# Kernel optimization log

Hardware: AMD Instinct MI355X
Metric: run time of the kernel (lower is better)

Reference implementation:

```python
import jax, jax.numpy as jnp
import numpy as np
from jax import lax

N_SEEDS = 16
N_SAMPS = 32
IN_C = 3
HID = [32, 64, 64]
K = 3
H = W = 64
EPS = 1e-5


def _uniform(key, shape, bound):
    return jax.random.uniform(key, shape, jnp.float32, -bound, bound)


def setup_inputs() -> dict:
    key = jax.random.key(0)
    keys = jax.random.split(key, 32)
    inp = {"x": jax.random.normal(keys[0], (N_SEEDS, N_SAMPS, IN_C, H, W), jnp.float32)}
    c_in = IN_C
    ki = 1
    for li, c_out in enumerate(HID, start=1):
        fan_in = c_in * K * K
        # kaiming_uniform with a=sqrt(5): gain=sqrt(2/(1+5))=sqrt(1/3); bound=sqrt(3)*gain/sqrt(fan)=1/sqrt(fan)
        wb = 1.0 / np.sqrt(fan_in)
        inp[f"w{li}"] = _uniform(keys[ki], (N_SEEDS * c_out, c_in, K, K), wb); ki += 1
        inp[f"b{li}"] = _uniform(keys[ki], (N_SEEDS * c_out,), wb); ki += 1
        inp[f"g{li}"] = jnp.ones((N_SEEDS * c_out,), jnp.float32)
        inp[f"be{li}"] = jnp.zeros((N_SEEDS * c_out,), jnp.float32)
        c_in = c_out
    return inp


def _layer(h, w, b, g, be):
    # grouped conv: groups = N_SEEDS, OIHW weights, NCHW data, stride 1, pad 1
    h = lax.conv_general_dilated(
        h, w, window_strides=(1, 1), padding=((1, 1), (1, 1)),
        feature_group_count=N_SEEDS,
        dimension_numbers=("NCHW", "OIHW", "NCHW"))
    h = h + b[None, :, None, None]
    # BatchNorm2d, training mode: batch statistics over (N, H, W), biased variance
    mean = jnp.mean(h, axis=(0, 2, 3))
    var = jnp.var(h, axis=(0, 2, 3))
    h = (h - mean[None, :, None, None]) * (g / jnp.sqrt(var + EPS))[None, :, None, None] + be[None, :, None, None]
    return jax.nn.relu(h)


def reference(x, w1, b1, g1, be1, w2, b2, g2, be2, w3, b3, g3, be3):
    S, N, C, Hh, Ww = x.shape  # (n_seeds, n_samps, C, H, W)
    h = jnp.swapaxes(x, 0, 1).reshape(N, S * C, Hh, Ww)
    h = _layer(h, w1, b1, g1, be1)
    h = _layer(h, w2, b2, g2, be2)
    h = _layer(h, w3, b3, g3, be3)
    c_out = HID[-1]
    h = h.reshape(N, S, c_out, Hh, Ww)
    return jnp.swapaxes(h, 0, 1)  # (n_seeds, n_samps, C_out, H, W)
```

## Files before the change

kernel.cpp:

```cpp
#include <hip/hip_runtime.h>
#include <cstddef>
#include <cstdint>

typedef __attribute__((ext_vector_type(8))) _Float16 half8;
typedef __attribute__((ext_vector_type(4))) _Float16 half4;
typedef __attribute__((ext_vector_type(4))) float f32x4;
typedef _Float16 half_t;

#define NS 16
#define NN 32

static const size_t OFF_H1P = 0;
static const size_t OFF_H3  = 138412032ull;
static const size_t OFF_ZR1 = 138412032ull + 276824064ull;
static const size_t OFF_ZR2 = OFF_ZR1 + 67584ull;
static const size_t OFF_WT1 = OFF_ZR2 + 135168ull;
static const size_t OFF_WT2 = OFF_WT1 + 55296ull;
static const size_t OFF_WT3 = OFF_WT2 + 589824ull;
static const size_t OFF_SUMS = OFF_WT3 + 1179648ull;
static const size_t OFF_PRM = OFF_SUMS + 20480ull;
static const size_t OFF_TH  = OFF_PRM + 30720ull;

static __device__ __forceinline__ half8 sr8(half8 v, half8 t) {
    half8 r = v + t;
    half8 z = {};
#if defined(__has_builtin) && __has_builtin(__builtin_elementwise_max)
    return __builtin_elementwise_max(r, z);
#else
#pragma unroll
    for (int j = 0; j < 8; ++j) r[j] = r[j] > (_Float16)0 ? r[j] : (_Float16)0;
    return r;
#endif
}

__global__ __launch_bounds__(256) void transform1_k(
    const float* __restrict__ w1, float* __restrict__ wt1)
{
    int idx = blockIdx.x * 256 + threadIdx.x;
    if (idx >= 13824) return;
    int o = idx & 31, tap = (idx >> 5) % 9, ic = (idx / 288) % 3, s = idx / 864;
    wt1[idx] = w1[((s * 32 + o) * 3 + ic) * 9 + tap];
}

__global__ __launch_bounds__(256) void wtrans2_k(
    const float* __restrict__ w2, const float* __restrict__ a1, half_t* __restrict__ wt2)
{
    int idx = blockIdx.x * 256 + threadIdx.x;
    if (idx >= 294912) return;
    int ic = idx & 31, oc = (idx >> 5) & 63, tap = (idx >> 11) % 9, s = idx / 18432;
    wt2[idx] = (half_t)(w2[((s * 64 + oc) * 32 + ic) * 9 + tap] * a1[s * 32 + ic]);
}

__global__ __launch_bounds__(256) void wtrans3_k(
    const float* __restrict__ w3, const float* __restrict__ a2, half_t* __restrict__ wt3)
{
    int idx = blockIdx.x * 256 + threadIdx.x;
    if (idx >= 589824) return;
    int ic = idx & 63, oc = (idx >> 6) & 63, tap = (idx >> 12) % 9, s = idx / 36864;
    wt3[idx] = (half_t)(w3[((s * 64 + oc) * 64 + ic) * 9 + tap] * a2[s * 64 + ic]);
}

__global__ __launch_bounds__(256) void conv1_k(
    const float* __restrict__ x, const float* __restrict__ wt1,
    const float* __restrict__ b1, half_t* __restrict__ h1p,
    float* __restrict__ sums1)
{
    __shared__ float smem[8512];
    float* xt = smem;
    float* bounce = smem;
    float* statsl = smem + 8448;
    const int tile = blockIdx.x, s = blockIdx.y, n = blockIdx.z;
    const int tx = tile & 3, ty = tile >> 2, tid = threadIdx.x;

    for (int i = tid; i < 972; i += 256) {
        int ic = i / 324, rem = i - ic * 324;
        int py = rem / 18, px = rem - py * 18;
        int gy = ty * 16 + py - 1, gx = tx * 16 + px - 1;
        float v = 0.f;
        if ((unsigned)gy < 64u && (unsigned)gx < 64u)
            v = x[(size_t)(((s * NN + n) * 3 + ic) * 64 + gy) * 64 + gx];
        xt[i] = v;
    }
    if (tid < 64) statsl[tid] = 0.f;
    __syncthreads();

    const int px = tid & 15, py = tid >> 4;
    float acc[32];
#pragma unroll
    for (int o = 0; o < 32; ++o) acc[o] = 0.f;
#pragma unroll
    for (int ic = 0; ic < 3; ++ic)
#pragma unroll
        for (int ky = 0; ky < 3; ++ky)
#pragma unroll
            for (int kx = 0; kx < 3; ++kx) {
                float v = xt[ic * 324 + (py + ky) * 18 + px + kx];
                const float* wp = wt1 + ((s * 3 + ic) * 9 + ky * 3 + kx) * 32;
#pragma unroll
                for (int o = 0; o < 32; ++o) acc[o] = fmaf(wp[o], v, acc[o]);
            }
    const float* bp = b1 + s * 32;
#pragma unroll
    for (int o = 0; o < 32; ++o) acc[o] += bp[o];

    const int gy1 = ty * 16 + py, gxp = tx * 16 + px + 1;
    half8* dst = (half8*)(h1p + (size_t)(n * NS + s) * 135168 + (size_t)(gy1 * 66 + gxp) * 32);
#pragma unroll
    for (int k = 0; k < 4; ++k) {
        half8 v8;
#pragma unroll
        for (int j = 0; j < 8; ++j) v8[j] = (half_t)acc[k * 8 + j];
        dst[k] = v8;
    }
    __syncthreads();
#pragma unroll
    for (int o = 0; o < 32; ++o) bounce[tid * 33 + o] = acc[o];
    __syncthreads();
    {
        const int oc = tid & 31, grp = tid >> 5;
        float s1 = 0.f, s2 = 0.f;
#pragma unroll 4
        for (int jj = 0; jj < 32; ++jj) {
            float v = bounce[(grp * 32 + jj) * 33 + oc];
            s1 += v; s2 += v * v;
        }
        atomicAdd(&statsl[oc * 2], s1);
        atomicAdd(&statsl[oc * 2 + 1], s2);
    }
    __syncthreads();
    if (tid < 64)
        atomicAdd(&sums1[(s * 32 + (tid >> 1)) * 2 + (tid & 1)], statsl[tid]);
}

__global__ void bnparam_k(const float* __restrict__ sums, const float* __restrict__ g,
                          const float* __restrict__ be, float* __restrict__ a,
                          float* __restrict__ b, float* __restrict__ t,
                          half_t* __restrict__ th, int C)
{
    int ch = blockIdx.x * 256 + threadIdx.x;
    if (ch >= C) return;
    const float inv = 1.f / 131072.f;
    float mean = sums[ch * 2] * inv;
    float var = sums[ch * 2 + 1] * inv - mean * mean;
    float sc = g[ch] * rsqrtf(var + 1e-5f);
    a[ch] = sc;
    float bb = be[ch] - mean * sc;
    b[ch] = bb;
    float tt = bb / sc;
    t[ch] = tt;
    th[ch] = (half_t)tt;
}

__global__ __launch_bounds__(256) void padfill_k(
    half_t* __restrict__ img, half_t* __restrict__ zrow, const float* __restrict__ t,
    int C, int c8shift, long imgstride, int rowstride, long tot_cols, long tot)
{
    long idx = (long)blockIdx.x * 256 + threadIdx.x;
    if (idx >= tot) return;
    const int nc8m = (1 << c8shift) - 1;
    if (idx < tot_cols) {
        int c8 = (int)idx & nc8m; long r = idx >> c8shift;
        int side = (int)r & 1; r >>= 1;
        int y = (int)r & 63; r >>= 6;
        int si = (int)(r & 15); int ni = (int)(r >> 4);
        half8 q;
#pragma unroll
        for (int j = 0; j < 8; ++j) q[j] = (half_t)(-(t[si * C + c8 * 8 + j] + 1.0f));
        *(half8*)(img + (long)(ni * NS + si) * imgstride + (long)y * rowstride +
                  (side ? 65 : 0) * C + c8 * 8) = q;
    } else {
        long r2 = idx - tot_cols;
        int c8 = (int)r2 & nc8m; r2 >>= c8shift;
        int xx = (int)(r2 % 66); int si = (int)(r2 / 66);
        half8 q;
#pragma unroll
        for (int j = 0; j < 8; ++j) q[j] = (half_t)(-(t[si * C + c8 * 8 + j] + 1.0f));
        *(half8*)(zrow + ((long)(si * 66 + xx)) * C + c8 * 8) = q;
    }
}

__device__ __forceinline__ void loadB2(half8 bf[4], const half_t* wb, int tap, int l15, int g) {
#pragma unroll
    for (int nt = 0; nt < 4; ++nt)
        bf[nt] = *(const half8*)(wb + (tap * 64 + nt * 16 + l15) * 32 + g * 8);
}

__device__ __forceinline__ void comp2(f32x4 acc[4][4], const half8 bf[4], const char* smem,
                                      int tap, int wv, int l15, int g) {
    const int ky = tap / 3, kx = tap - ky * 3;
#pragma unroll
    for (int mt = 0; mt < 4; ++mt) {
        int p = (wv * 4 + mt + ky) * 18 + l15 + kx;
        half8 av = *(const half8*)(smem + p * 80 + g * 16);
#pragma unroll
        for (int nt = 0; nt < 4; ++nt)
            acc[mt][nt] = __builtin_amdgcn_mfma_f32_16x16x32_f16(av, bf[nt], acc[mt][nt], 0, 0, 0);
    }
}

__global__ __launch_bounds__(256, 3) void conv2_k(
    const half_t* __restrict__ h1p, const half_t* __restrict__ zr1,
    const half_t* __restrict__ wt2, const float* __restrict__ b2,
    const half_t* __restrict__ th1, half_t* __restrict__ h2p,
    float* __restrict__ sums2)
{
    __shared__ __align__(16) char smem[37376];
    float* statsl = (float*)(smem + 36864);
    const int tile = blockIdx.x, s = blockIdx.y, n = blockIdx.z;
    const int tx = tile & 3, ty = tile >> 2, tid = threadIdx.x;
    const int l = tid & 63, wv = tid >> 6, l15 = l & 15, g = l >> 4;
    if (tid < 128) statsl[tid] = 0.f;

    const half_t* wb = wt2 + (size_t)s * 18432;
    half8 bfa[4], bfb[4];
    loadB2(bfa, wb, 0, l15, g);

    const half_t* img = h1p + (size_t)(n * NS + s) * 135168;
    const half_t* zrow = zr1 + s * 2112;
    const int j = tid & 3;
    const half8 tshj = *(const half8*)(th1 + s * 32 + j * 8);
    for (int i = tid; i < 1296; i += 256) {
        int p = i >> 2;
        int py = p / 18, pxx = p - py * 18;
        int gy = ty * 16 + py - 1;
        const half_t* rp = ((unsigned)gy < 64u) ? (img + (size_t)gy * 2112) : zrow;
        half8 v = sr8(*(const half8*)(rp + (tx * 16 + pxx) * 32 + j * 8), tshj);
        *(half8*)(smem + p * 80 + j * 16) = v;
    }
    __syncthreads();

    f32x4 acc[4][4];
#pragma unroll
    for (int mt = 0; mt < 4; ++mt)
#pragma unroll
        for (int nt = 0; nt < 4; ++nt) acc[mt][nt] = (f32x4){0.f, 0.f, 0.f, 0.f};

#pragma unroll
    for (int tap = 0; tap < 9; ++tap) {
        if (tap & 1) {
            if (tap < 8) loadB2(bfa, wb, tap + 1, l15, g);
            comp2(acc, bfb, smem, tap, wv, l15, g);
        } else {
            if (tap < 8) loadB2(bfb, wb, tap + 1, l15, g);
            comp2(acc, bfa, smem, tap, wv, l15, g);
        }
    }

    float s1a[4], s2a[4];
#pragma unroll
    for (int nt = 0; nt < 4; ++nt) {
        float bias = b2[s * 64 + nt * 16 + l15];
        float s1 = 0.f, s2 = 0.f;
#pragma unroll
        for (int mt = 0; mt < 4; ++mt)
#pragma unroll
            for (int r = 0; r < 4; ++r) {
                float v = acc[mt][nt][r] + bias;
                acc[mt][nt][r] = v;
                s1 += v; s2 += v * v;
            }
        s1 += __shfl_xor(s1, 16); s1 += __shfl_xor(s1, 32);
        s2 += __shfl_xor(s2, 16); s2 += __shfl_xor(s2, 32);
        s1a[nt] = s1; s2a[nt] = s2;
    }
    if (l < 16) {
#pragma unroll
        for (int nt = 0; nt < 4; ++nt) {
            atomicAdd(&statsl[(nt * 16 + l15) * 2], s1a[nt]);
            atomicAdd(&statsl[(nt * 16 + l15) * 2 + 1], s2a[nt]);
        }
    }
    __syncthreads();

    half_t* obuf = (half_t*)smem;
#pragma unroll
    for (int mt = 0; mt < 4; ++mt)
#pragma unroll
        for (int nt = 0; nt < 4; ++nt)
#pragma unroll
            for (int r = 0; r < 4; ++r)
                obuf[((wv * 4 + mt) * 16 + g * 4 + r) * 72 + nt * 16 + l15] = (half_t)acc[mt][nt][r];
    __syncthreads();

    half_t* img2 = h2p + (size_t)(n * NS + s) * 270336;
    for (int i = tid; i < 2048; i += 256) {
        int p = i >> 3, cc = i & 7;
        int y = ty * 16 + (p >> 4), xp = tx * 16 + (p & 15) + 1;
        *(half8*)(img2 + (size_t)y * 4224 + xp * 64 + cc * 8) = *(const half8*)(obuf + p * 72 + cc * 8);
    }
    if (tid < 128)
        atomicAdd(&sums2[(s * 64 + (tid >> 1)) * 2 + (tid & 1)], statsl[tid]);
}

__global__ __launch_bounds__(512, 4) void conv3_k(
    const half_t* __restrict__ h2p, const half_t* __restrict__ zr2,
    const half_t* __restrict__ wt3, const float* __restrict__ b3,
    const half_t* __restrict__ th2, half_t* __restrict__ h3,
    float* __restrict__ sums3)
{
    __shared__ __align__(16) char smem[51200];
    float* statsl = (float*)(smem + 50688);
    const int ty = blockIdx.x, s = blockIdx.y, n = blockIdx.z;
    const int tid = threadIdx.x;
    const int l = tid & 63, w = tid >> 6, l15 = l & 15, g = l >> 4;
    const int wy = w & 3, och = w >> 2;
    const int ty4 = ty * 4;
    if (tid < 128) statsl[tid] = 0.f;

    const half_t* img = h2p + (size_t)(n * NS + s) * 270336;
    const half_t* zrow = zr2 + s * 4224;
    const half_t* wb = wt3 + (size_t)s * 36864;
    const int j = tid & 7;
    const half8 tshj = *(const half8*)(th2 + s * 64 + j * 8);

    half8 sa0, sa1, sa2, sa3, sa4; int aa0, aa1, aa2, aa3, aa4;
#define PREPA(K, ST, SL) { int idx = tid + K * 512; int p = idx >> 3; int rr = p / 66; \
    int col = p - rr * 66; int row = ty4 - 1 + rr; bool ok = idx < 2112; \
    const half_t* rp = ((unsigned)row < 64u) ? (img + (size_t)row * 4224) : zrow; \
    ST = *(const half8*)(rp + col * 64 + j * 8); \
    SL = ok ? (rr * 8448 + col * 128 + ((j * 16) ^ ((col & 7) << 4))) : -1; }
    PREPA(0, sa0, aa0)
    PREPA(1, sa1, aa1)
    PREPA(2, sa2, aa2)
    PREPA(3, sa3, aa3)
    PREPA(4, sa4, aa4)
#undef PREPA
    half8 sb0, sb1, sb2; int ab0, ab1, ab2;
#define PREPB(K, ST, SL) { int idx = tid + K * 512; int p = idx >> 3; int rr = p / 66; \
    int col = p - rr * 66; int row = ty4 + 3 + rr; bool ok = idx < 1056; \
    const half_t* rp = ((unsigned)row < 64u) ? (img + (size_t)row * 4224) : zrow; \
    ST = *(const half8*)(rp + col * 64 + j * 8); \
    SL = ok ? ((4 + rr) * 8448 + col * 128 + ((j * 16) ^ ((col & 7) << 4))) : -1; }
    PREPB(0, sb0, ab0)
    PREPB(1, sb1, ab1)
    PREPB(2, sb2, ab2)
#undef PREPB
    if (aa0 >= 0) *(half8*)(smem + aa0) = sr8(sa0, tshj);
    if (aa1 >= 0) *(half8*)(smem + aa1) = sr8(sa1, tshj);
    if (aa2 >= 0) *(half8*)(smem + aa2) = sr8(sa2, tshj);
    if (aa3 >= 0) *(half8*)(smem + aa3) = sr8(sa3, tshj);
    if (aa4 >= 0) *(half8*)(smem + aa4) = sr8(sa4, tshj);
    __syncthreads();

    f32x4 acc[4][2];
#pragma unroll
    for (int mt = 0; mt < 4; ++mt)
#pragma unroll
        for (int nt = 0; nt < 2; ++nt) acc[mt][nt] = (f32x4){0.f, 0.f, 0.f, 0.f};

    const int UT[19] = {0,1,2,0,1,2, 3,4,5,6,7,8, 3,4,5,6,7,8, 0};
    const int UK[19] = {0,0,0,1,1,1, 0,0,0,0,0,0, 1,1,1,1,1,1, 0};
    half8 bfa[2], bfb[2], bfc[2];
#define LW3(BF, U) { \
    BF[0] = *(const half8*)(wb + (UT[U] * 64 + och * 32 + l15) * 64 + UK[U] * 32 + g * 8); \
    BF[1] = *(const half8*)(wb + (UT[U] * 64 + och * 32 + 16 + l15) * 64 + UK[U] * 32 + g * 8); }
    LW3(bfa, 0)
    LW3(bfb, 1)
#define CSTEP3(BF, U) { \
    int tap_ = UT[U]; int ky_ = tap_ / 3, kx_ = tap_ - ky_ * 3; \
    const char* rp_ = smem + (wy + ky_) * 8448; \
    _Pragma("unroll") \
    for (int mt = 0; mt < 4; ++mt) { \
        int px = mt * 16 + l15 + kx_; \
        int sw = (px & 7) << 4; \
        half8 a_ = *(const half8*)(rp_ + px * 128 + ((UK[U] * 64 + g * 16) ^ sw)); \
        acc[mt][0] = __builtin_amdgcn_mfma_f32_16x16x32_f16(a_, BF[0], acc[mt][0], 0, 0, 0); \
        acc[mt][1] = __builtin_amdgcn_mfma_f32_16x16x32_f16(a_, BF[1], acc[mt][1], 0, 0, 0); \
    } }

    LW3(bfc, 2)  CSTEP3(bfa, 0)
    LW3(bfa, 3)  CSTEP3(bfb, 1)
    LW3(bfb, 4)  CSTEP3(bfc, 2)
    LW3(bfc, 5)  CSTEP3(bfa, 3)
    LW3(bfa, 6)  CSTEP3(bfb, 4)
    LW3(bfb, 7)  CSTEP3(bfc, 5)
    if (ab0 >= 0) *(half8*)(smem + ab0) = sr8(sb0, tshj);
    if (ab1 >= 0) *(half8*)(smem + ab1) = sr8(sb1, tshj);
    if (ab2 >= 0) *(half8*)(smem + ab2) = sr8(sb2, tshj);
    __syncthreads();
    LW3(bfc, 8)   CSTEP3(bfa, 6)
    LW3(bfa, 9)   CSTEP3(bfb, 7)
    LW3(bfb, 10)  CSTEP3(bfc, 8)
    LW3(bfc, 11)  CSTEP3(bfa, 9)
    LW3(bfa, 12)  CSTEP3(bfb, 10)
    LW3(bfb, 13)  CSTEP3(bfc, 11)
    LW3(bfc, 14)  CSTEP3(bfa, 12)
    LW3(bfa, 15)  CSTEP3(bfb, 13)
    LW3(bfb, 16)  CSTEP3(bfc, 14)
    LW3(bfc, 17)  CSTEP3(bfa, 15)
                  CSTEP3(bfb, 16)
                  CSTEP3(bfc, 17)
#undef CSTEP3
#undef LW3

    float bias0 = b3[s * 64 + och * 32 + l15];
    float bias1 = b3[s * 64 + och * 32 + 16 + l15];
    float s10 = 0.f, s20 = 0.f, s11 = 0.f, s21 = 0.f;
    const int gy = ty4 + wy;
    half_t* hb = h3 + (size_t)((s * NN + n) * 64) * 4096;
#pragma unroll
    for (int mt = 0; mt < 4; ++mt)
#pragma unroll
        for (int nt = 0; nt < 2; ++nt) {
            int c = och * 32 + nt * 16 + l15;
            float bias = nt ? bias1 : bias0;
            half4 hv;
#pragma unroll
            for (int r = 0; r < 4; ++r) {
                float vv = acc[mt][nt][r] + bias;
                hv[r] = (half_t)vv;
                if (nt) { s11 += vv; s21 += vv * vv; } else { s10 += vv; s20 += vv * vv; }
            }
            *(half4*)(hb + (size_t)c * 4096 + gy * 64 + mt * 16 + g * 4) = hv;
        }

    s10 += __shfl_xor(s10, 16); s10 += __shfl_xor(s10, 32);
    s20 += __shfl_xor(s20, 16); s20 += __shfl_xor(s20, 32);
    s11 += __shfl_xor(s11, 16); s11 += __shfl_xor(s11, 32);
    s21 += __shfl_xor(s21, 16); s21 += __shfl_xor(s21, 32);
    if (l < 16) {
        atomicAdd(&statsl[(och * 32 + l15) * 2], s10);
        atomicAdd(&statsl[(och * 32 + l15) * 2 + 1], s20);
        atomicAdd(&statsl[(och * 32 + 16 + l15) * 2], s11);
        atomicAdd(&statsl[(och * 32 + 16 + l15) * 2 + 1], s21);
    }
    __syncthreads();
    if (tid < 128)
        atomicAdd(&sums3[(s * 64 + (tid >> 1)) * 2 + (tid & 1)], statsl[tid]);
}

__global__ __launch_bounds__(256) void final_k(float* __restrict__ out,
                                               const half_t* __restrict__ h3,
                                               const float* __restrict__ a3,
                                               const float* __restrict__ b3p)
{
    const size_t stride = (size_t)gridDim.x * 256;
    for (size_t i = (size_t)blockIdx.x * 256 + threadIdx.x; i < 16777216ull; i += stride) {
        size_t e = i * 8;
        int ch = (int)((e >> 12) & 63) + (int)(e >> 23) * 64;
        float sc = a3[ch], sh = b3p[ch];
        half8 hv = *(const half8*)(h3 + e);
        f32x4 v0, v1;
#pragma unroll
        for (int r = 0; r < 4; ++r) {
            v0[r] = fmaxf(fmaf(sc, (float)hv[r], sh), 0.f);
            v1[r] = fmaxf(fmaf(sc, (float)hv[r + 4], sh), 0.f);
        }
        *(f32x4*)(out + e) = v0;
        *(f32x4*)(out + e + 4) = v1;
    }
}

extern "C" void kernel_launch(void* const* d_in, const int* in_sizes, int n_in,
                              void* d_out, int out_size, void* d_ws, size_t ws_size,
                              hipStream_t stream)
{
    const float* x   = (const float*)d_in[0];
    const float* w1  = (const float*)d_in[1];
    const float* b1  = (const float*)d_in[2];
    const float* g1  = (const float*)d_in[3];
    const float* be1 = (const float*)d_in[4];
    const float* w2  = (const float*)d_in[5];
    const float* b2  = (const float*)d_in[6];
    const float* g2  = (const float*)d_in[7];
    const float* be2 = (const float*)d_in[8];
    const float* w3  = (const float*)d_in[9];
    const float* b3  = (const float*)d_in[10];
    const float* g3  = (const float*)d_in[11];
    const float* be3 = (const float*)d_in[12];

    char* ws = (char*)d_ws;
    half_t* h1p = (half_t*)(ws + OFF_H1P);
    half_t* h2p = (half_t*)d_out;
    half_t* h3  = (half_t*)(ws + OFF_H3);
    half_t* zr1 = (half_t*)(ws + OFF_ZR1);
    half_t* zr2 = (half_t*)(ws + OFF_ZR2);
    float*  wt1 = (float*)(ws + OFF_WT1);
    half_t* wt2 = (half_t*)(ws + OFF_WT2);
    half_t* wt3 = (half_t*)(ws + OFF_WT3);
    float*  sums = (float*)(ws + OFF_SUMS);
    float *s1v = sums, *s2v = sums + 1024, *s3v = sums + 3072;
    float*  prm = (float*)(ws + OFF_PRM);
    float *a1 = prm,        *b1p = prm + 512,  *t1 = prm + 1024;
    float *a2 = prm + 1536, *b2p = prm + 2560, *t2 = prm + 3584;
    float *a3 = prm + 4608, *b3p = prm + 5632, *t3 = prm + 6656;
    half_t* th = (half_t*)(ws + OFF_TH);
    half_t *th1 = th, *th2 = th + 512, *th3 = th + 1536;
    float* out = (float*)d_out;

    hipMemsetAsync(ws + OFF_SUMS, 0, 20480, stream);
    transform1_k<<<54, 256, 0, stream>>>(w1, wt1);
    dim3 grid1(16, 16, 32);
    conv1_k<<<grid1, 256, 0, stream>>>(x, wt1, b1, h1p, s1v);
    bnparam_k<<<2, 256, 0, stream>>>(s1v, g1, be1, a1, b1p, t1, th1, 512);
    padfill_k<<<1041, 256, 0, stream>>>(h1p, zr1, t1, 32, 2, 135168L, 2112, 262144L, 266368L);
    wtrans2_k<<<1152, 256, 0, stream>>>(w2, a1, wt2);
    conv2_k<<<grid1, 256, 0, stream>>>(h1p, zr1, wt2, b2, th1, h2p, s2v);
    bnparam_k<<<4, 256, 0, stream>>>(s2v, g2, be2, a2, b2p, t2, th2, 1024);
    padfill_k<<<2081, 256, 0, stream>>>(h2p, zr2, t2, 64, 3, 270336L, 4224, 524288L, 532736L);
    wtrans3_k<<<2304, 256, 0, stream>>>(w3, a2, wt3);
    dim3 grid3(16, 16, 32);
    conv3_k<<<grid3, 512, 0, stream>>>(h2p, zr2, wt3, b3, th2, h3, s3v);
    bnparam_k<<<4, 256, 0, stream>>>(s3v, g3, be3, a3, b3p, t3, th3, 1024);
    final_k<<<4096, 256, 0, stream>>>(out, h3, a3, b3p);
}
```

Before: 848.4 us.

## Pipeline conv3 over 16-row strips with async global-to-LDS ring buffer

conv3 now handles a 16-row strip per block, four 4-row steps in all, instead of one 4-row tile. Input rows stream into a 9-row LDS ring through global_load_lds direct copies that overlap the MFMA work. The XOR swizzle moves into the global h2 layout (conv2 stores and padfill) so the raw 16-byte copies land already swizzled, and the BN shift plus ReLU is applied when the data is read from LDS. This cuts halo reloads and register staging, at the cost of more LDS per block (lower occupancy), fewer blocks, and repeated sr8 work on every A-fragment read.

```diff
diff --git a/kernel.cpp b/kernel.cpp
--- a/kernel.cpp
+++ b/kernel.cpp
@@ -31,6 +31,22 @@
     for (int j = 0; j < 8; ++j) r[j] = r[j] > (_Float16)0 ? r[j] : (_Float16)0;
     return r;
 #endif
+}
+
+typedef __attribute__((address_space(1))) const void gas_t;
+typedef __attribute__((address_space(3))) void las_t;
+static __device__ __forceinline__ void gl16(const void* g, void* l) {
+    __builtin_amdgcn_global_load_lds((gas_t*)g, (las_t*)l, 16, 0, 0);
+}
+
+static __device__ __forceinline__ void stage_row3(const half_t* __restrict__ img,
+                                                  const half_t* __restrict__ zrow,
+                                                  char* smem, int r, int w, int lane) {
+    const char* src = (const char*)(((unsigned)r < 64u) ? (img + (size_t)r * 4224) : zrow)
+                      + (size_t)w * 1056;
+    char* dst = smem + (size_t)((unsigned)(r + 18) % 9u) * 8448 + w * 1056;
+    gl16(src + lane * 16, dst + lane * 16);
+    if (lane < 2) gl16(src + 1024 + lane * 16, dst + 1024 + lane * 16);
 }
 
 __global__ __launch_bounds__(256) void transform1_k(
@@ -153,7 +169,7 @@
 
 __global__ __launch_bounds__(256) void padfill_k(
     half_t* __restrict__ img, half_t* __restrict__ zrow, const float* __restrict__ t,
-    int C, int c8shift, long imgstride, int rowstride, long tot_cols, long tot)
+    int C, int c8shift, long imgstride, int rowstride, long tot_cols, long tot, int swz)
 {
     long idx = (long)blockIdx.x * 256 + threadIdx.x;
     if (idx >= tot) return;
@@ -166,8 +182,10 @@
         half8 q;
 #pragma unroll
         for (int j = 0; j < 8; ++j) q[j] = (half_t)(-(t[si * C + c8 * 8 + j] + 1.0f));
+        int col = side ? 65 : 0;
+        int off = swz ? ((c8 * 8) ^ ((col & 7) << 3)) : (c8 * 8);
         *(half8*)(img + (long)(ni * NS + si) * imgstride + (long)y * rowstride +
-                  (side ? 65 : 0) * C + c8 * 8) = q;
+                  col * C + off) = q;
     } else {
         long r2 = idx - tot_cols;
         int c8 = (int)r2 & nc8m; r2 >>= c8shift;
@@ -175,7 +193,8 @@
         half8 q;
 #pragma unroll
         for (int j = 0; j < 8; ++j) q[j] = (half_t)(-(t[si * C + c8 * 8 + j] + 1.0f));
-        *(half8*)(zrow + ((long)(si * 66 + xx)) * C + c8 * 8) = q;
+        int off = swz ? ((c8 * 8) ^ ((xx & 7) << 3)) : (c8 * 8);
+        *(half8*)(zrow + ((long)(si * 66 + xx)) * C + off) = q;
     }
 }
 
@@ -286,7 +305,8 @@
     for (int i = tid; i < 2048; i += 256) {
         int p = i >> 3, cc = i & 7;
         int y = ty * 16 + (p >> 4), xp = tx * 16 + (p & 15) + 1;
-        *(half8*)(img2 + (size_t)y * 4224 + xp * 64 + cc * 8) = *(const half8*)(obuf + p * 72 + cc * 8);
+        *(half8*)(img2 + (size_t)y * 4224 + xp * 64 + ((cc * 8) ^ ((xp & 7) << 3))) =
+            *(const half8*)(obuf + p * 72 + cc * 8);
     }
     if (tid < 128)
         atomicAdd(&sums2[(s * 64 + (tid >> 1)) * 2 + (tid & 1)], statsl[tid]);
@@ -298,121 +318,125 @@
     const half_t* __restrict__ th2, half_t* __restrict__ h3,
     float* __restrict__ sums3)
 {
-    __shared__ __align__(16) char smem[51200];
-    float* statsl = (float*)(smem + 50688);
-    const int ty = blockIdx.x, s = blockIdx.y, n = blockIdx.z;
+    __shared__ __align__(16) char smem[76544];
+    float* statsl = (float*)(smem + 76032);
+    const int strip = blockIdx.x, s = blockIdx.y, n = blockIdx.z;
     const int tid = threadIdx.x;
     const int l = tid & 63, w = tid >> 6, l15 = l & 15, g = l >> 4;
     const int wy = w & 3, och = w >> 2;
-    const int ty4 = ty * 4;
+    const int yb = strip * 16;
     if (tid < 128) statsl[tid] = 0.f;
 
     const half_t* img = h2p + (size_t)(n * NS + s) * 270336;
     const half_t* zrow = zr2 + s * 4224;
     const half_t* wb = wt3 + (size_t)s * 36864;
-    const int j = tid & 7;
-    const half8 tshj = *(const half8*)(th2 + s * 64 + j * 8);
-
-    half8 sa0, sa1, sa2, sa3, sa4; int aa0, aa1, aa2, aa3, aa4;
-#define PREPA(K, ST, SL) { int idx = tid + K * 512; int p = idx >> 3; int rr = p / 66; \
-    int col = p - rr * 66; int row = ty4 - 1 + rr; bool ok = idx < 2112; \
-    const half_t* rp = ((unsigned)row < 64u) ? (img + (size_t)row * 4224) : zrow; \
-    ST = *(const half8*)(rp + col * 64 + j * 8); \
-    SL = ok ? (rr * 8448 + col * 128 + ((j * 16) ^ ((col & 7) << 4))) : -1; }
-    PREPA(0, sa0, aa0)
-    PREPA(1, sa1, aa1)
-    PREPA(2, sa2, aa2)
-    PREPA(3, sa3, aa3)
-    PREPA(4, sa4, aa4)
-#undef PREPA
-    half8 sb0, sb1, sb2; int ab0, ab1, ab2;
-#define PREPB(K, ST, SL) { int idx = tid + K * 512; int p = idx >> 3; int rr = p / 66; \
-    int col = p - rr * 66; int row = ty4 + 3 + rr; bool ok = idx < 1056; \
-    const half_t* rp = ((unsigned)row < 64u) ? (img + (size_t)row * 4224) : zrow; \
-    ST = *(const half8*)(rp + col * 64 + j * 8); \
-    SL = ok ? ((4 + rr) * 8448 + col * 128 + ((j * 16) ^ ((col & 7) << 4))) : -1; }
-    PREPB(0, sb0, ab0)
-    PREPB(1, sb1, ab1)
-    PREPB(2, sb2, ab2)
-#undef PREPB
-    if (aa0 >= 0) *(half8*)(smem + aa0) = sr8(sa0, tshj);
-    if (aa1 >= 0) *(half8*)(smem + aa1) = sr8(sa1, tshj);
-    if (aa2 >= 0) *(half8*)(smem + aa2) = sr8(sa2, tshj);
-    if (aa3 >= 0) *(half8*)(smem + aa3) = sr8(sa3, tshj);
-    if (aa4 >= 0) *(half8*)(smem + aa4) = sr8(sa4, tshj);
-    __syncthreads();
-
-    f32x4 acc[4][2];
-#pragma unroll
-    for (int mt = 0; mt < 4; ++mt)
-#pragma unroll
-        for (int nt = 0; nt < 2; ++nt) acc[mt][nt] = (f32x4){0.f, 0.f, 0.f, 0.f};
-
-    const int UT[19] = {0,1,2,0,1,2, 3,4,5,6,7,8, 3,4,5,6,7,8, 0};
-    const int UK[19] = {0,0,0,1,1,1, 0,0,0,0,0,0, 1,1,1,1,1,1, 0};
-    half8 bfa[2], bfb[2], bfc[2];
-#define LW3(BF, U) { \
-    BF[0] = *(const half8*)(wb + (UT[U] * 64 + och * 32 + l15) * 64 + UK[U] * 32 + g * 8); \
-    BF[1] = *(const half8*)(wb + (UT[U] * 64 + och * 32 + 16 + l15) * 64 + UK[U] * 32 + g * 8); }
-    LW3(bfa, 0)
-    LW3(bfb, 1)
-#define CSTEP3(BF, U) { \
-    int tap_ = UT[U]; int ky_ = tap_ / 3, kx_ = tap_ - ky_ * 3; \
-    const char* rp_ = smem + (wy + ky_) * 8448; \
+    const half8 tsh0 = *(const half8*)(th2 + s * 64 + g * 8);
+    const half8 tsh1 = *(const half8*)(th2 + s * 64 + 32 + g * 8);
+
+    const int UT[18] = {0,1,2,0,1,2, 3,4,5,6,7,8, 3,4,5,6,7,8};
+    const int UK[18] = {0,0,0,1,1,1, 0,0,0,0,0,0, 1,1,1,1,1,1};
+    half8 wAa,wAb,wBa,wBb,wCa,wCb,wDa,wDb,wEa,wEb,wFa,wFb;
+#define LWQ(W, U) { \
+    W##a = *(const half8*)(wb + (UT[U]*64 + och*32 + l15)*64 + UK[U]*32 + g*8); \
+    W##b = *(const half8*)(wb + (UT[U]*64 + och*32 + 16 + l15)*64 + UK[U]*32 + g*8); }
+#define CS(W, U) { \
+    const char* rp_ = (UT[U] < 3) ? rp0 : (UT[U] < 6) ? rp1 : rp2; \
+    const int kx_ = UT[U] % 3; \
+    const half8 tsh_ = UK[U] ? tsh1 : tsh0; \
     _Pragma("unroll") \
     for (int mt = 0; mt < 4; ++mt) { \
-        int px = mt * 16 + l15 + kx_; \
+        int px = mt*16 + l15 + kx_; \
         int sw = (px & 7) << 4; \
-        half8 a_ = *(const half8*)(rp_ + px * 128 + ((UK[U] * 64 + g * 16) ^ sw)); \
-        acc[mt][0] = __builtin_amdgcn_mfma_f32_16x16x32_f16(a_, BF[0], acc[mt][0], 0, 0, 0); \
-        acc[mt][1] = __builtin_amdgcn_mfma_f32_16x16x32_f16(a_, BF[1], acc[mt][1], 0, 0, 0); \
+        half8 a_ = sr8(*(const half8*)(rp_ + px*128 + ((UK[U]*64 + g*16) ^ sw)), tsh_); \
+        acc[mt][0] = __builtin_amdgcn_mfma_f32_16x16x32_f16(a_, W##a, acc[mt][0], 0, 0, 0); \
+        acc[mt][1] = __builtin_amdgcn_mfma_f32_16x16x32_f16(a_, W##b, acc[mt][1], 0, 0, 0); \
     } }
 
-    LW3(bfc, 2)  CSTEP3(bfa, 0)
-    LW3(bfa, 3)  CSTEP3(bfb, 1)
-    LW3(bfb, 4)  CSTEP3(bfc, 2)
-    LW3(bfc, 5)  CSTEP3(bfa, 3)
-    LW3(bfa, 6)  CSTEP3(bfb, 4)
-    LW3(bfb, 7)  CSTEP3(bfc, 5)
-    if (ab0 >= 0) *(half8*)(smem + ab0) = sr8(sb0, tshj);
-    if (ab1 >= 0) *(half8*)(smem + ab1) = sr8(sb1, tshj);
-    if (ab2 >= 0) *(half8*)(smem + ab2) = sr8(sb2, tshj);
-    __syncthreads();
-    LW3(bfc, 8)   CSTEP3(bfa, 6)
-    LW3(bfa, 9)   CSTEP3(bfb, 7)
-    LW3(bfb, 10)  CSTEP3(bfc, 8)
-    LW3(bfc, 11)  CSTEP3(bfa, 9)
-    LW3(bfa, 12)  CSTEP3(bfb, 10)
-    LW3(bfb, 13)  CSTEP3(bfc, 11)
-    LW3(bfc, 14)  CSTEP3(bfa, 12)
-    LW3(bfa, 15)  CSTEP3(bfb, 13)
-    LW3(bfb, 16)  CSTEP3(bfc, 14)
-    LW3(bfc, 17)  CSTEP3(bfa, 15)
-                  CSTEP3(bfb, 16)
-                  CSTEP3(bfc, 17)
-#undef CSTEP3
-#undef LW3
-
-    float bias0 = b3[s * 64 + och * 32 + l15];
-    float bias1 = b3[s * 64 + och * 32 + 16 + l15];
+    LWQ(wA,0) LWQ(wB,1) LWQ(wC,2) LWQ(wD,3) LWQ(wE,4) LWQ(wF,5)
+    __builtin_amdgcn_sched_barrier(0);
+
+    for (int r = yb - 1; r <= yb + 7; ++r)
+        stage_row3(img, zrow, smem, r, w, l);
+    __builtin_amdgcn_sched_barrier(0);
+    asm volatile("s_waitcnt vmcnt(6)" ::: "memory");
+    __builtin_amdgcn_s_barrier();
+    __builtin_amdgcn_sched_barrier(0);
+
+    const float bias0 = b3[s * 64 + och * 32 + l15];
+    const float bias1 = b3[s * 64 + och * 32 + 16 + l15];
     float s10 = 0.f, s20 = 0.f, s11 = 0.f, s21 = 0.f;
-    const int gy = ty4 + wy;
     half_t* hb = h3 + (size_t)((s * NN + n) * 64) * 4096;
-#pragma unroll
-    for (int mt = 0; mt < 4; ++mt)
-#pragma unroll
-        for (int nt = 0; nt < 2; ++nt) {
-            int c = och * 32 + nt * 16 + l15;
-            float bias = nt ? bias1 : bias0;
-            half4 hv;
-#pragma unroll
-            for (int r = 0; r < 4; ++r) {
-                float vv = acc[mt][nt][r] + bias;
-                hv[r] = (half_t)vv;
-                if (nt) { s11 += vv; s21 += vv * vv; } else { s10 += vv; s20 += vv * vv; }
+
+#pragma unroll 1
+    for (int t = 0; t < 4; ++t) {
+        const int rb = yb + 4 * t;
+        const int r0 = rb + wy - 1;
+        const char* rp0 = smem + (size_t)((unsigned)(r0 + 18) % 9u) * 8448;
+        const char* rp1 = smem + (size_t)((unsigned)(r0 + 19) % 9u) * 8448;
+        const char* rp2 = smem + (size_t)((unsigned)(r0 + 20) % 9u) * 8448;
+
+        f32x4 acc[4][2];
+#pragma unroll
+        for (int mt = 0; mt < 4; ++mt)
+#pragma unroll
+            for (int nt = 0; nt < 2; ++nt) acc[mt][nt] = (f32x4){0.f, 0.f, 0.f, 0.f};
+
+        CS(wA,0)   LWQ(wA,6)
+        CS(wB,1)   LWQ(wB,7)
+        CS(wC,2)   LWQ(wC,8)
+        CS(wD,3)   LWQ(wD,9)
+        CS(wE,4)   LWQ(wE,10)
+        CS(wF,5)   LWQ(wF,11)
+        CS(wA,6)   LWQ(wA,12)
+        CS(wB,7)   LWQ(wB,13)
+        CS(wC,8)   LWQ(wC,14)
+        CS(wD,9)   LWQ(wD,15)
+        CS(wE,10)  LWQ(wE,16)
+        CS(wF,11)  LWQ(wF,17)
+        CS(wA,12)  LWQ(wA,0)
+        CS(wB,13)  LWQ(wB,1)
+        CS(wC,14)  LWQ(wC,2)
+        CS(wD,15)  LWQ(wD,3)
+        CS(wE,16)  LWQ(wE,4)
+        CS(wF,17)  LWQ(wF,5)
+
+        const int gy = rb + wy;
+#pragma unroll
+        for (int mt = 0; mt < 4; ++mt)
+#pragma unroll
+            for (int nt = 0; nt < 2; ++nt) {
+                int c = och * 32 + nt * 16 + l15;
+                float bias = nt ? bias1 : bias0;
+                half4 hv;
+#pragma unroll
+                for (int r = 0; r < 4; ++r) {
+                    float vv = acc[mt][nt][r] + bias;
+                    hv[r] = (half_t)vv;
+                    if (nt) { s11 += vv; s21 += vv * vv; } else { s10 += vv; s20 += vv * vv; }
+                }
+                *(half4*)(hb + (size_t)c * 4096 + gy * 64 + mt * 16 + g * 4) = hv;
             }
-            *(half4*)(hb + (size_t)c * 4096 + gy * 64 + mt * 16 + g * 4) = hv;
+
+        __builtin_amdgcn_sched_barrier(0);
+        asm volatile("s_waitcnt lgkmcnt(0)" ::: "memory");
+        __builtin_amdgcn_s_barrier();
+        __builtin_amdgcn_sched_barrier(0);
+        if (t < 3) {
+            stage_row3(img, zrow, smem, rb + 8, w, l);
+            if (t < 2) {
+                stage_row3(img, zrow, smem, rb + 9, w, l);
+                stage_row3(img, zrow, smem, rb + 10, w, l);
+                stage_row3(img, zrow, smem, rb + 11, w, l);
+            }
+            __builtin_amdgcn_sched_barrier(0);
+            if (t < 2) asm volatile("s_waitcnt vmcnt(6)" ::: "memory");
+            else       asm volatile("s_waitcnt vmcnt(0)" ::: "memory");
+            __builtin_amdgcn_s_barrier();
+            __builtin_amdgcn_sched_barrier(0);
         }
+    }
+#undef CS
+#undef LWQ
 
     s10 += __shfl_xor(s10, 16); s10 += __shfl_xor(s10, 32);
     s20 += __shfl_xor(s20, 16); s20 += __shfl_xor(s20, 32);
@@ -493,13 +517,13 @@
     dim3 grid1(16, 16, 32);
     conv1_k<<<grid1, 256, 0, stream>>>(x, wt1, b1, h1p, s1v);
     bnparam_k<<<2, 256, 0, stream>>>(s1v, g1, be1, a1, b1p, t1, th1, 512);
-    padfill_k<<<1041, 256, 0, stream>>>(h1p, zr1, t1, 32, 2, 135168L, 2112, 262144L, 266368L);
+    padfill_k<<<1041, 256, 0, stream>>>(h1p, zr1, t1, 32, 2, 135168L, 2112, 262144L, 266368L, 0);
     wtrans2_k<<<1152, 256, 0, stream>>>(w2, a1, wt2);
     conv2_k<<<grid1, 256, 0, stream>>>(h1p, zr1, wt2, b2, th1, h2p, s2v);
     bnparam_k<<<4, 256, 0, stream>>>(s2v, g2, be2, a2, b2p, t2, th2, 1024);
-    padfill_k<<<2081, 256, 0, stream>>>(h2p, zr2, t2, 64, 3, 270336L, 4224, 524288L, 532736L);
+    padfill_k<<<2081, 256, 0, stream>>>(h2p, zr2, t2, 64, 3, 270336L, 4224, 524288L, 532736L, 1);
     wtrans3_k<<<2304, 256, 0, stream>>>(w3, a2, wt3);
-    dim3 grid3(16, 16, 32);
+    dim3 grid3(4, 16, 32);
     conv3_k<<<grid3, 512, 0, stream>>>(h2p, zr2, wt3, b3, th2, h3, s3v);
     bnparam_k<<<4, 256, 0, stream>>>(s3v, g3, be3, a3, b3p, t3, th3, 1024);
     final_k<<<4096, 256, 0, stream>>>(out, h3, a3, b3p);
```

Result: slower. 1.153 ms (+35.9%).
